# Optimization experiments

Hardware: AMD Instinct MI355X
Metric: run time of the kernel (lower is better)

The kernel has to match this reference:

```python
import jax, jax.numpy as jnp
import numpy as np

EPS = 1e-8
LN_EPS = 1e-5
CAPACITY_BETA = 1.5
IDEAL_CLASSES = 5.0

B, F, E, H, C, G = 8192, 1024, 30, 256, 100, 4096


def setup_inputs() -> dict:
    key = jax.random.key(0)
    ks = jax.random.split(key, 8)
    x = jax.random.normal(ks[0], (B, F), dtype=jnp.float32)
    prototypes = jax.random.normal(ks[1], (E, F), dtype=jnp.float32)
    g_new = jax.random.normal(ks[2], (G,), dtype=jnp.float32)
    g_mem = jax.random.normal(ks[3], (E, G), dtype=jnp.float32)
    class_counts = jax.random.randint(ks[4], (E,), 0, 12, dtype=jnp.int32)
    W1 = jax.random.normal(ks[5], (E, F, H), dtype=jnp.float32) * (1.0 / np.sqrt(F))
    b1 = jnp.zeros((E, H), dtype=jnp.float32)
    gamma = jnp.ones((E, H), dtype=jnp.float32)
    beta = jnp.zeros((E, H), dtype=jnp.float32)
    W2 = jax.random.normal(ks[6], (E, H, C), dtype=jnp.float32) * (1.0 / np.sqrt(H))
    b2 = jnp.zeros((E, C), dtype=jnp.float32)
    return {"x": x, "prototypes": prototypes, "g_new": g_new, "g_mem": g_mem,
            "class_counts": class_counts, "W1": W1, "b1": b1, "gamma": gamma,
            "beta": beta, "W2": W2, "b2": b2}


def _route_scores(x, prototypes, g_new, g_mem, class_counts):
    # Cosine similarity of each sample to each expert prototype: [B, E]
    xn = x / (jnp.linalg.norm(x, axis=-1, keepdims=True) + EPS)
    pn = prototypes / (jnp.linalg.norm(prototypes, axis=-1, keepdims=True) + EPS)
    sim = xn @ pn.T
    # Gradient alignment score per expert (cosine of new grad vs EMA memory), mapped to [0, 1]
    gn = g_new / (jnp.linalg.norm(g_new) + EPS)
    gm = g_mem / (jnp.linalg.norm(g_mem, axis=-1, keepdims=True) + EPS)
    align = 0.5 * (1.0 + gm @ gn)  # [E]
    # Capacity penalty: exponential decay once an expert exceeds its ideal class load
    overload = jnp.maximum(class_counts.astype(jnp.float32) / IDEAL_CLASSES - 1.0, 0.0)
    capacity = jnp.exp(-CAPACITY_BETA * overload)  # [E]
    return sim * (align * capacity)[None, :]  # [B, E]


def reference(x, prototypes, g_new, g_mem, class_counts, W1, b1, gamma, beta, W2, b2):
    scores = _route_scores(x, prototypes, g_new, g_mem, class_counts)  # [B, E]
    assign = jnp.argmax(scores, axis=-1)  # [B] expert id per sample
    # Expert MLP: Linear -> LayerNorm -> GELU -> Linear, evaluated for all experts
    h = jnp.einsum('bf,efh->ebh', x, W1) + b1[:, None, :]  # [E, B, H]
    mu = h.mean(axis=-1, keepdims=True)
    var = ((h - mu) ** 2).mean(axis=-1, keepdims=True)
    ln = (h - mu) * jax.lax.rsqrt(var + LN_EPS) * gamma[:, None, :] + beta[:, None, :]
    a = jax.nn.gelu(ln, approximate=False)  # torch nn.GELU default is exact erf
    logits_all = jnp.einsum('ebh,ehc->ebc', a, W2) + b2[:, None, :]  # [E, B, C]
    # Dispatch: each sample keeps only its assigned expert's logits
    logits = logits_all[assign, jnp.arange(x.shape[0])]  # [B, C]
    return logits
```

## Files before the change

### kernel.cpp

```cpp
#include <hip/hip_runtime.h>
#include <hip/hip_bf16.h>
#include <math.h>
#include <float.h>

namespace {
constexpr int Bn = 8192;
constexpr int Fn = 1024;
constexpr int En = 30;
constexpr int Hn = 256;
constexpr int Cn = 100;
constexpr int Gn = 4096;
constexpr int TILECAP64 = 158;
constexpr int TILECAP16 = 540;
constexpr float EPSF  = 1e-8f;
constexpr float LNEPS = 1e-5f;

typedef _Float16 f16x8 __attribute__((ext_vector_type(8)));
typedef __fp16   h16x2 __attribute__((ext_vector_type(2)));
typedef float    f32x4 __attribute__((ext_vector_type(4)));

__device__ __forceinline__ int bswz(int k) { return (k & 7) ^ ((k >> 3) << 2); }

__device__ __forceinline__ f16x8 pk8(const float* v) {
  union { h16x2 h2[4]; f16x8 v8; } u;
#pragma unroll
  for (int i = 0; i < 4; i++)
    u.h2[i] = __builtin_amdgcn_cvt_pkrtz(v[2 * i], v[2 * i + 1]);
  return u.v8;
}
}

#define GLDS16(g, s) __builtin_amdgcn_global_load_lds(                         \
    (const __attribute__((address_space(1))) void*)(uintptr_t)(g),             \
    (__attribute__((address_space(3))) void*)(uintptr_t)(s), 16, 0, 0)

__global__ __launch_bounds__(256) void k_route_w(
    const float* __restrict__ protos,
    const float* __restrict__ g_new,
    const float* __restrict__ g_mem,
    const int* __restrict__ ccounts,
    float* __restrict__ w,
    int* __restrict__ cnt) {
  const int e = blockIdx.x, t = threadIdx.x;
  if (e == 0 && t < 32) cnt[t] = 0;
  float d = 0.f, gm2 = 0.f, gn2 = 0.f, p2 = 0.f;
  for (int g = t; g < Gn; g += 256) {
    float a = g_new[g];
    float m = g_mem[(size_t)e * Gn + g];
    d += a * m; gm2 += m * m; gn2 += a * a;
  }
  for (int f = t; f < Fn; f += 256) {
    float v = protos[(size_t)e * Fn + f];
    p2 += v * v;
  }
#pragma unroll
  for (int m = 1; m < 64; m <<= 1) {
    d   += __shfl_xor(d, m);
    gm2 += __shfl_xor(gm2, m);
    gn2 += __shfl_xor(gn2, m);
    p2  += __shfl_xor(p2, m);
  }
  __shared__ float red[4][4];
  const int lane = t & 63, wid = t >> 6;
  if (lane == 0) { red[wid][0] = d; red[wid][1] = gm2; red[wid][2] = gn2; red[wid][3] = p2; }
  __syncthreads();
  if (t == 0) {
    d   = red[0][0] + red[1][0] + red[2][0] + red[3][0];
    gm2 = red[0][1] + red[1][1] + red[2][1] + red[3][1];
    gn2 = red[0][2] + red[1][2] + red[2][2] + red[3][2];
    p2  = red[0][3] + red[1][3] + red[2][3] + red[3][3];
    float align = 0.5f * (1.0f + d / ((sqrtf(gm2) + EPSF) * (sqrtf(gn2) + EPSF)));
    float over  = fmaxf((float)ccounts[e] / 5.0f - 1.0f, 0.0f);
    float cap   = expf(-1.5f * over);
    w[e] = align * cap / (sqrtf(p2) + EPSF);
  }
}

__global__ __launch_bounds__(256) void k_scores_mfma(
    const float* __restrict__ x,
    const float* __restrict__ protos,
    const float* __restrict__ w,
    int* __restrict__ assign,
    float* __restrict__ hbuf) {
  const int b0 = blockIdx.x * 16;
  extern __shared__ char smem[];
  __shared__ float av_[16][2];
  __shared__ int   ai_[16][2];
  const int t = threadIdx.x, l = t & 63, wv = t >> 6;
  const int nt = wv & 1;

  {
    float* hz = hbuf + (size_t)blockIdx.x * 4096 + t * 4;
#pragma unroll
    for (int k = 0; k < 4; k++)
      *(float4*)(hz + k * 1024) = make_float4(0.f, 0.f, 0.f, 0.f);
  }

  const char* asrc;
  {
    const int row = t >> 4, pos = t & 15;
    asrc = (const char*)x + (size_t)(b0 + row) * 4096 + (pos ^ (row & 7)) * 16;
  }
  const char* bsrc[2];
#pragma unroll
  for (int i = 0; i < 2; i++) {
    const int D = i * 256 + t, row = D >> 4, pos = D & 15;
    bsrc[i] = (const char*)protos + (size_t)min(row, En - 1) * 4096 +
              (pos ^ (row & 7)) * 16;
  }

  const int r15 = l & 15, kq = l >> 4;
  int addrA[2][2];
#pragma unroll
  for (int ks = 0; ks < 2; ks++)
#pragma unroll
    for (int i = 0; i < 2; i++)
      addrA[ks][i] = r15 * 256 + (((ks * 8 + kq * 2 + i) ^ (r15 & 7)) * 16);
  int addrB[2][2];
#pragma unroll
  for (int ks = 0; ks < 2; ks++)
#pragma unroll
    for (int i = 0; i < 2; i++) {
      const int er = nt * 16 + r15;
      addrB[ks][i] = 4096 + er * 256 + (((ks * 8 + kq * 2 + i) ^ (er & 7)) * 16);
    }

  const int  e_w   = nt * 16 + r15;
  const bool valid = (e_w < En);
  const float wsc  = w[min(e_w, En - 1)];

  f32x4 acc = (f32x4){0.f, 0.f, 0.f, 0.f};

  auto stage = [&](int buf, int kt) {
    char* bb = smem + buf * 12288;
    GLDS16(asrc + kt * 256, bb + wv * 1024);
#pragma unroll
    for (int i = 0; i < 2; i++)
      GLDS16(bsrc[i] + kt * 256, bb + 4096 + i * 4096 + wv * 1024);
  };

  stage(0, 0);
  __syncthreads();
  int cur = 0;
  for (int kt = 0; kt < 16; ++kt) {
    if (kt < 15) stage(cur ^ 1, kt + 1);
    const char* bb = smem + cur * 12288;
    if (wv < 2) {
#pragma unroll
      for (int ks = 0; ks < 2; ks++) {
        f16x8 ah, al;
        {
          float4 a0 = *(const float4*)(bb + addrA[ks][0]);
          float4 a1 = *(const float4*)(bb + addrA[ks][1]);
          float av[8] = {a0.x, a0.y, a0.z, a0.w, a1.x, a1.y, a1.z, a1.w};
#pragma unroll
          for (int j = 0; j < 8; j++) {
            _Float16 hh = (_Float16)av[j];
            ah[j] = hh;
            al[j] = (_Float16)(av[j] - (float)hh);
          }
        }
        f16x8 bh, bl;
        {
          float4 b0v = *(const float4*)(bb + addrB[ks][0]);
          float4 b1v = *(const float4*)(bb + addrB[ks][1]);
          float bv[8] = {b0v.x, b0v.y, b0v.z, b0v.w, b1v.x, b1v.y, b1v.z, b1v.w};
#pragma unroll
          for (int j = 0; j < 8; j++) {
            _Float16 hh = (_Float16)bv[j];
            bh[j] = hh;
            bl[j] = (_Float16)(bv[j] - (float)hh);
          }
        }
        acc = __builtin_amdgcn_mfma_f32_16x16x32_f16(ah, bh, acc, 0, 0, 0);
        acc = __builtin_amdgcn_mfma_f32_16x16x32_f16(al, bh, acc, 0, 0, 0);
        acc = __builtin_amdgcn_mfma_f32_16x16x32_f16(ah, bl, acc, 0, 0, 0);
        acc = __builtin_amdgcn_mfma_f32_16x16x32_f16(al, bl, acc, 0, 0, 0);
      }
    }
    __syncthreads();
    cur ^= 1;
  }

  if (wv < 2) {
#pragma unroll
    for (int j = 0; j < 4; j++) {
      float best = valid ? acc[j] * wsc : -FLT_MAX;
      int bi = e_w;
#pragma unroll
      for (int m = 1; m < 16; m <<= 1) {
        float ov = __shfl_xor(best, m);
        int   oi = __shfl_xor(bi, m);
        if (ov > best || (ov == best && oi < bi)) { best = ov; bi = oi; }
      }
      if (r15 == 0) {
        const int s = kq * 4 + j;
        av_[s][nt] = best;
        ai_[s][nt] = bi;
      }
    }
  }
  __syncthreads();
  if (t < 16) {
    const float v0 = av_[t][0], v1 = av_[t][1];
    assign[b0 + t] = (v1 > v0) ? ai_[t][1] : ai_[t][0];
  }
}

__global__ __launch_bounds__(256) void k_bucket(
    const int* __restrict__ assign,
    int* __restrict__ cnt,
    int* __restrict__ list) {
  __shared__ int lcnt[32], lbase[32];
  const int t = threadIdx.x;
  const int b = blockIdx.x * 256 + t;
  if (t < 32) lcnt[t] = 0;
  __syncthreads();
  const int e = assign[b];
  const int lpos = atomicAdd(&lcnt[e], 1);
  __syncthreads();
  if (t < 32) lbase[t] = (lcnt[t] > 0) ? atomicAdd(&cnt[t], lcnt[t]) : 0;
  __syncthreads();
  list[e * Bn + lbase[e] + lpos] = b;
}

__global__ void k_plan(const int* __restrict__ cnt,
                       int* __restrict__ tiles64,
                       int* __restrict__ tiles16) {
  const int t = threadIdx.x;
  if (t == 0) {
    int tot = 0;
    for (int e = 0; e < En; e++) {
      int nt = (cnt[e] + 63) >> 6;
      for (int k = 0; k < nt && tot + k < TILECAP64; k++)
        tiles64[tot + k] = (e << 16) | k;
      tot += nt;
    }
    for (int k = tot; k < TILECAP64; k++) tiles64[k] = -1;
  } else if (t == 1) {
    int tot = 0;
    for (int e = 0; e < En; e++) {
      int nt = (cnt[e] + 15) >> 4;
      for (int k = 0; k < nt && tot + k < TILECAP16; k++)
        tiles16[tot + k] = (e << 16) | k;
      tot += nt;
    }
    for (int k = tot; k < TILECAP16; k++) tiles16[k] = -1;
  }
}

__global__ __launch_bounds__(256) void k_l1_f16(
    const float* __restrict__ x,
    const float* __restrict__ W1,
    const float* __restrict__ b1,
    const int* __restrict__ cnt,
    const int* __restrict__ list,
    const int* __restrict__ tiles,
    float* __restrict__ hbuf) {
  const int tv = tiles[blockIdx.x];
  if (tv < 0) return;
  const int e = tv >> 16, ti = tv & 0xffff;
  const int n = cnt[e];
  const int s0 = ti * 64;
  const int ns = min(64, n - s0);
  const int h0 = blockIdx.y * 128;
  const int k0 = blockIdx.z * 16;

  extern __shared__ char smem[];
  __shared__ int idx[64];
  const int t = threadIdx.x, l = t & 63, w = t >> 6;
  if (t < 64) idx[t] = list[e * Bn + s0 + min(t, ns - 1)];
  __syncthreads();

  const char* asrc[2];
#pragma unroll
  for (int i = 0; i < 2; i++) {
    const int D = i * 256 + t, row = D >> 3, pos = D & 7;
    asrc[i] = (const char*)x + (size_t)idx[row] * 4096 + (pos ^ (row & 7)) * 16;
  }
  const char* bsrc[4];
#pragma unroll
  for (int i = 0; i < 4; i++) {
    const int k  = i * 8 + w * 2 + (l >> 5);
    const int c  = (l & 31) ^ bswz(k);
    bsrc[i] = (const char*)W1 +
              ((size_t)(e * Fn + k) * Hn + h0) * 4 + c * 16;
  }

  const int r15 = l & 15, kq = l >> 4;
  int addrA[4][2];
#pragma unroll
  for (int m = 0; m < 4; m++)
#pragma unroll
    for (int i = 0; i < 2; i++) {
      const int row = m * 16 + r15;
      addrA[m][i] = row * 128 + (((kq * 2 + i) ^ (row & 7)) * 16);
    }
  int addrB[2][8];
#pragma unroll
  for (int nn = 0; nn < 2; nn++)
#pragma unroll
    for (int j = 0; j < 8; j++) {
      const int h = w * 32 + nn * 16 + r15;
      const int kl = kq * 8 + j;
      addrB[nn][j] = 8192 + kl * 512 + (((h >> 2) ^ bswz(kl)) * 16) + (h & 3) * 4;
    }

  f32x4 acc[4][2];
#pragma unroll
  for (int m = 0; m < 4; m++)
#pragma unroll
    for (int nn = 0; nn < 2; nn++) acc[m][nn] = (f32x4){0.f, 0.f, 0.f, 0.f};

  auto stage = [&](int buf, int kt) {
    char* bb = smem + buf * 24576;
#pragma unroll
    for (int i = 0; i < 2; i++)
      GLDS16(asrc[i] + kt * 128, bb + i * 4096 + w * 1024);
#pragma unroll
    for (int i = 0; i < 4; i++)
      GLDS16(bsrc[i] + (size_t)kt * 32768, bb + 8192 + i * 4096 + w * 1024);
  };

  stage(0, k0);
  __syncthreads();
  int cur = 0;
  for (int kt = k0; kt < k0 + 16; ++kt) {
    if (kt < k0 + 15) stage(cur ^ 1, kt + 1);
    const char* bb = smem + cur * 24576;

    f16x8 ah[4], al[4];
#pragma unroll
    for (int m = 0; m < 4; m++) {
      float4 a0 = *(const float4*)(bb + addrA[m][0]);
      float4 a1 = *(const float4*)(bb + addrA[m][1]);
      float av[8] = {a0.x, a0.y, a0.z, a0.w, a1.x, a1.y, a1.z, a1.w};
#pragma unroll
      for (int j = 0; j < 8; j++) {
        _Float16 hh = (_Float16)av[j];
        ah[m][j] = hh;
        al[m][j] = (_Float16)(av[j] - (float)hh);
      }
    }
#pragma unroll
    for (int nn = 0; nn < 2; nn++) {
      float bv[8];
#pragma unroll
      for (int j = 0; j < 8; j++)
        bv[j] = *(const float*)(bb + addrB[nn][j]);
      const f16x8 bh = pk8(bv);
#pragma unroll
      for (int m = 0; m < 4; m++) {
        acc[m][nn] = __builtin_amdgcn_mfma_f32_16x16x32_f16(ah[m], bh, acc[m][nn], 0, 0, 0);
        acc[m][nn] = __builtin_amdgcn_mfma_f32_16x16x32_f16(al[m], bh, acc[m][nn], 0, 0, 0);
      }
    }
    __syncthreads();
    cur ^= 1;
  }

  float bias[2];
#pragma unroll
  for (int nn = 0; nn < 2; nn++)
    bias[nn] = (blockIdx.z == 0)
             ? b1[(size_t)e * Hn + h0 + w * 32 + nn * 16 + r15] : 0.f;
#pragma unroll
  for (int m = 0; m < 4; m++) {
#pragma unroll
    for (int j = 0; j < 4; j++) {
      const int r = m * 16 + kq * 4 + j;
      if (r < ns) {
        float* dst = hbuf + (size_t)idx[r] * Hn + h0 + w * 32;
#pragma unroll
        for (int nn = 0; nn < 2; nn++)
          atomicAdd(dst + nn * 16 + r15, acc[m][nn][j] + bias[nn]);
      }
    }
  }
}

__global__ __launch_bounds__(256) void k_ln2_mfma(
    const float* __restrict__ hbuf,
    const float* __restrict__ gamma,
    const float* __restrict__ beta,
    const float* __restrict__ W2,
    const float* __restrict__ b2,
    const int* __restrict__ cnt,
    const int* __restrict__ list,
    const int* __restrict__ tiles16,
    float* __restrict__ out) {
  const int tv = tiles16[blockIdx.x];
  if (tv < 0) return;
  const int e = tv >> 16, ti = tv & 0xffff;
  const int n = cnt[e];
  const int s0 = ti * 16;
  const int ns = min(16, n - s0);

  __shared__ __align__(16) char aT[16 * 1024];
  __shared__ __align__(16) char bW[2][13312];
  __shared__ int idx[16];

  const int t = threadIdx.x, l = t & 63, w = t >> 6;
  if (t < 16) idx[t] = list[e * Bn + s0 + min(t, ns - 1)];

  const char* w2e = (const char*)W2 + (size_t)e * (Hn * Cn * 4);
  auto stageB = [&](int buf, int kt) {
    const int base = kt * 12800;
    for (int i = w; i < 13; i += 4) {
      int off = base + i * 1024 + l * 16;
      if (off > 102400 - 16) off = 102400 - 16;
      GLDS16(w2e + off, bW[buf] + i * 1024);
    }
  };

  stageB(0, 0);
  __syncthreads();

  const int s = t >> 4, seg = t & 15;
  const int b = idx[s];
  float hv[16];
  float sum = 0.f, sq = 0.f;
  {
    const float* src = hbuf + (size_t)b * Hn + seg * 16;
#pragma unroll
    for (int i = 0; i < 16; i += 4) {
      float4 v = *(const float4*)(src + i);
      hv[i] = v.x; hv[i+1] = v.y; hv[i+2] = v.z; hv[i+3] = v.w;
      sum += v.x + v.y + v.z + v.w;
      sq  += v.x*v.x + v.y*v.y + v.z*v.z + v.w*v.w;
    }
  }
#pragma unroll
  for (int m = 1; m < 16; m <<= 1) { sum += __shfl_xor(sum, m); sq += __shfl_xor(sq, m); }
  const float mu = sum * (1.f / 256.f);
  float var = fmaxf(sq * (1.f / 256.f) - mu * mu, 0.f);
  const float rstd = rsqrtf(var + LNEPS);
#pragma unroll
  for (int i4 = 0; i4 < 4; i4++) {
    float av[4];
#pragma unroll
    for (int j = 0; j < 4; j++) {
      const int hh = seg * 16 + i4 * 4 + j;
      const float g  = gamma[(size_t)e * Hn + hh];
      const float be = beta[(size_t)e * Hn + hh];
      const float ln = (hv[i4 * 4 + j] - mu) * rstd * g + be;
      av[j] = 0.5f * ln * (1.0f + erff(ln * 0.70710678118654752f));
    }
    const int chunk = (seg * 4 + i4) ^ (s & 7);
    *(float4*)(aT + s * 1024 + chunk * 16) = make_float4(av[0], av[1], av[2], av[3]);
  }

  const int r15 = l & 15, kq = l >> 4;
  int addrB[2][8];
#pragma unroll
  for (int ni = 0; ni < 2; ni++) {
    const int nt = w + ni * 4;
    const int c = nt * 16 + r15;
#pragma unroll
    for (int j = 0; j < 8; j++)
      addrB[ni][j] = ((kq * 8 + j) * Cn + c) * 4;
  }

  f32x4 acc[2];
  acc[0] = (f32x4){0.f, 0.f, 0.f, 0.f};
  acc[1] = (f32x4){0.f, 0.f, 0.f, 0.f};

  __syncthreads();

  int cur = 0;
  for (int kt = 0; kt < 8; ++kt) {
    if (kt < 7) stageB(cur ^ 1, kt + 1);

    f16x8 ah, al;
    {
      const int c0 = (kt * 8 + kq * 2) ^ (r15 & 7);
      const int c1 = (kt * 8 + kq * 2 + 1) ^ (r15 & 7);
      float4 a0 = *(const float4*)(aT + r15 * 1024 + c0 * 16);
      float4 a1 = *(const float4*)(aT + r15 * 1024 + c1 * 16);
      float av[8] = {a0.x, a0.y, a0.z, a0.w, a1.x, a1.y, a1.z, a1.w};
#pragma unroll
      for (int j = 0; j < 8; j++) {
        _Float16 hh = (_Float16)av[j];
        ah[j] = hh;
        al[j] = (_Float16)(av[j] - (float)hh);
      }
    }
#pragma unroll
    for (int ni = 0; ni < 2; ni++) {
      const int nt = w + ni * 4;
      if (nt < 7) {
        float bv[8];
#pragma unroll
        for (int j = 0; j < 8; j++)
          bv[j] = *(const float*)(bW[cur] + addrB[ni][j]);
        f16x8 bh, bl;
#pragma unroll
        for (int j = 0; j < 8; j++) {
          _Float16 hh = (_Float16)bv[j];
          bh[j] = hh;
          bl[j] = (_Float16)(bv[j] - (float)hh);
        }
        acc[ni] = __builtin_amdgcn_mfma_f32_16x16x32_f16(ah, bh, acc[ni], 0, 0, 0);
        acc[ni] = __builtin_amdgcn_mfma_f32_16x16x32_f16(al, bh, acc[ni], 0, 0, 0);
        acc[ni] = __builtin_amdgcn_mfma_f32_16x16x32_f16(ah, bl, acc[ni], 0, 0, 0);
      }
    }
    __syncthreads();
    cur ^= 1;
  }

#pragma unroll
  for (int ni = 0; ni < 2; ni++) {
    const int nt = w + ni * 4;
    if (nt >= 7) continue;
    const int c = nt * 16 + r15;
    if (c >= Cn) continue;
    const float bias = b2[(size_t)e * Cn + c];
#pragma unroll
    for (int j = 0; j < 4; j++) {
      const int r = kq * 4 + j;
      if (r < ns)
        out[(size_t)idx[r] * Cn + c] = acc[ni][j] + bias;
    }
  }
}

extern "C" void kernel_launch(void* const* d_in, const int* in_sizes, int n_in,
                              void* d_out, int out_size, void* d_ws, size_t ws_size,
                              hipStream_t stream) {
  const void* x       = d_in[0];
  const void* protos  = d_in[1];
  const void* g_new   = d_in[2];
  const void* g_mem   = d_in[3];
  const int*  ccounts = (const int*)d_in[4];
  const void* W1      = d_in[5];
  const void* b1      = d_in[6];
  const void* gamma   = d_in[7];
  const void* beta    = d_in[8];
  const void* W2      = d_in[9];
  const void* b2      = d_in[10];

  char* ws = (char*)d_ws;
  float* w       = (float*)(ws);
  int*   assign  = (int*)(ws + 512);
  int*   tiles64 = (int*)(ws + 512);
  int*   tiles16 = (int*)(ws + 512 + 1024);
  int*   cnt     = (int*)(ws + 512 + Bn * 4);
  int*   list    = (int*)(ws + 512 + Bn * 4 + 256);
  float* hbuf    = (float*)(ws + 1016576);

  k_route_w<<<dim3(En), 256, 0, stream>>>(
      (const float*)protos, (const float*)g_new, (const float*)g_mem,
      ccounts, w, cnt);
  k_scores_mfma<<<dim3(Bn / 16), 256, 24576, stream>>>(
      (const float*)x, (const float*)protos, w, assign, hbuf);
  k_bucket<<<Bn / 256, 256, 0, stream>>>(assign, cnt, list);
  k_plan<<<1, 64, 0, stream>>>(cnt, tiles64, tiles16);
  k_l1_f16<<<dim3(TILECAP64, 2, 2), 256, 49152, stream>>>(
      (const float*)x, (const float*)W1, (const float*)b1,
      cnt, list, tiles64, hbuf);
  k_ln2_mfma<<<dim3(TILECAP16), 256, 0, stream>>>(
      hbuf, (const float*)gamma, (const float*)beta, (const float*)W2,
      (const float*)b2, cnt, list, tiles16, (float*)d_out);
}
```

Baseline: 219.3 us.

## Fuse bucketing into scores kernel and split K across all four waves

The scores kernel now uses all four waves by splitting the feature dimension into two halves, each processed by a pair of waves, with a shared-memory reduction of the partial accumulators before the argmax. The separate bucketing kernel is removed: each block appends its 16 samples to per-expert lists with local and global atomics directly after computing assignments. This cuts one launch and the assign buffer round-trip and halves the serial K loop per block, at the cost of twice the shared memory per block (lower occupancy) and more global atomics on cnt, since there are far more blocks.

```diff
diff --git a/kernel.cpp b/kernel.cpp
--- a/kernel.cpp
+++ b/kernel.cpp
@@ -80,14 +80,19 @@
     const float* __restrict__ x,
     const float* __restrict__ protos,
     const float* __restrict__ w,
-    int* __restrict__ assign,
+    int* __restrict__ cnt,
+    int* __restrict__ list,
     float* __restrict__ hbuf) {
   const int b0 = blockIdx.x * 16;
   extern __shared__ char smem[];
   __shared__ float av_[16][2];
   __shared__ int   ai_[16][2];
+  __shared__ float pacc[2][64][4];
+  __shared__ int   lcnt[32], lbase[32];
   const int t = threadIdx.x, l = t & 63, wv = t >> 6;
-  const int nt = wv & 1;
+  const int nt = wv & 1, kh = wv >> 1;
+
+  if (t < 32) lcnt[t] = 0;
 
   {
     float* hz = hbuf + (size_t)blockIdx.x * 4096 + t * 4;
@@ -110,19 +115,21 @@
   }
 
   const int r15 = l & 15, kq = l >> 4;
+  const int khb = kh * 12288;
   int addrA[2][2];
 #pragma unroll
   for (int ks = 0; ks < 2; ks++)
 #pragma unroll
     for (int i = 0; i < 2; i++)
-      addrA[ks][i] = r15 * 256 + (((ks * 8 + kq * 2 + i) ^ (r15 & 7)) * 16);
+      addrA[ks][i] = khb + r15 * 256 + (((ks * 8 + kq * 2 + i) ^ (r15 & 7)) * 16);
   int addrB[2][2];
 #pragma unroll
   for (int ks = 0; ks < 2; ks++)
 #pragma unroll
     for (int i = 0; i < 2; i++) {
       const int er = nt * 16 + r15;
-      addrB[ks][i] = 4096 + er * 256 + (((ks * 8 + kq * 2 + i) ^ (er & 7)) * 16);
+      addrB[ks][i] = khb + 4096 + er * 256 +
+                     (((ks * 8 + kq * 2 + i) ^ (er & 7)) * 16);
     }
 
   const int  e_w   = nt * 16 + r15;
@@ -132,57 +139,67 @@
   f32x4 acc = (f32x4){0.f, 0.f, 0.f, 0.f};
 
   auto stage = [&](int buf, int kt) {
-    char* bb = smem + buf * 12288;
-    GLDS16(asrc + kt * 256, bb + wv * 1024);
+    char* bb = smem + buf * 24576;
+    const int ko = kt * 256;
+    GLDS16(asrc + ko,            bb + wv * 1024);
 #pragma unroll
     for (int i = 0; i < 2; i++)
-      GLDS16(bsrc[i] + kt * 256, bb + 4096 + i * 4096 + wv * 1024);
+      GLDS16(bsrc[i] + ko,       bb + 4096 + i * 4096 + wv * 1024);
+    GLDS16(asrc + 2048 + ko,     bb + 12288 + wv * 1024);
+#pragma unroll
+    for (int i = 0; i < 2; i++)
+      GLDS16(bsrc[i] + 2048 + ko, bb + 12288 + 4096 + i * 4096 + wv * 1024);
   };
 
   stage(0, 0);
   __syncthreads();
   int cur = 0;
-  for (int kt = 0; kt < 16; ++kt) {
-    if (kt < 15) stage(cur ^ 1, kt + 1);
-    const char* bb = smem + cur * 12288;
-    if (wv < 2) {
-#pragma unroll
-      for (int ks = 0; ks < 2; ks++) {
-        f16x8 ah, al;
-        {
-          float4 a0 = *(const float4*)(bb + addrA[ks][0]);
-          float4 a1 = *(const float4*)(bb + addrA[ks][1]);
-          float av[8] = {a0.x, a0.y, a0.z, a0.w, a1.x, a1.y, a1.z, a1.w};
-#pragma unroll
-          for (int j = 0; j < 8; j++) {
-            _Float16 hh = (_Float16)av[j];
-            ah[j] = hh;
-            al[j] = (_Float16)(av[j] - (float)hh);
-          }
+  for (int kt = 0; kt < 8; ++kt) {
+    if (kt < 7) stage(cur ^ 1, kt + 1);
+    const char* bb = smem + cur * 24576;
+#pragma unroll
+    for (int ks = 0; ks < 2; ks++) {
+      f16x8 ah, al;
+      {
+        float4 a0 = *(const float4*)(bb + addrA[ks][0]);
+        float4 a1 = *(const float4*)(bb + addrA[ks][1]);
+        float av[8] = {a0.x, a0.y, a0.z, a0.w, a1.x, a1.y, a1.z, a1.w};
+#pragma unroll
+        for (int j = 0; j < 8; j++) {
+          _Float16 hh = (_Float16)av[j];
+          ah[j] = hh;
+          al[j] = (_Float16)(av[j] - (float)hh);
         }
-        f16x8 bh, bl;
-        {
-          float4 b0v = *(const float4*)(bb + addrB[ks][0]);
-          float4 b1v = *(const float4*)(bb + addrB[ks][1]);
-          float bv[8] = {b0v.x, b0v.y, b0v.z, b0v.w, b1v.x, b1v.y, b1v.z, b1v.w};
-#pragma unroll
-          for (int j = 0; j < 8; j++) {
-            _Float16 hh = (_Float16)bv[j];
-            bh[j] = hh;
-            bl[j] = (_Float16)(bv[j] - (float)hh);
-          }
+      }
+      f16x8 bh, bl;
+      {
+        float4 b0v = *(const float4*)(bb + addrB[ks][0]);
+        float4 b1v = *(const float4*)(bb + addrB[ks][1]);
+        float bv[8] = {b0v.x, b0v.y, b0v.z, b0v.w, b1v.x, b1v.y, b1v.z, b1v.w};
+#pragma unroll
+        for (int j = 0; j < 8; j++) {
+          _Float16 hh = (_Float16)bv[j];
+          bh[j] = hh;
+          bl[j] = (_Float16)(bv[j] - (float)hh);
         }
-        acc = __builtin_amdgcn_mfma_f32_16x16x32_f16(ah, bh, acc, 0, 0, 0);
-        acc = __builtin_amdgcn_mfma_f32_16x16x32_f16(al, bh, acc, 0, 0, 0);
-        acc = __builtin_amdgcn_mfma_f32_16x16x32_f16(ah, bl, acc, 0, 0, 0);
-        acc = __builtin_amdgcn_mfma_f32_16x16x32_f16(al, bl, acc, 0, 0, 0);
-      }
+      }
+      acc = __builtin_amdgcn_mfma_f32_16x16x32_f16(ah, bh, acc, 0, 0, 0);
+      acc = __builtin_amdgcn_mfma_f32_16x16x32_f16(al, bh, acc, 0, 0, 0);
+      acc = __builtin_amdgcn_mfma_f32_16x16x32_f16(ah, bl, acc, 0, 0, 0);
+      acc = __builtin_amdgcn_mfma_f32_16x16x32_f16(al, bl, acc, 0, 0, 0);
     }
     __syncthreads();
     cur ^= 1;
   }
 
-  if (wv < 2) {
+  if (kh == 1) {
+#pragma unroll
+    for (int j = 0; j < 4; j++) pacc[nt][l][j] = acc[j];
+  }
+  __syncthreads();
+  if (kh == 0) {
+#pragma unroll
+    for (int j = 0; j < 4; j++) acc[j] += pacc[nt][l][j];
 #pragma unroll
     for (int j = 0; j < 4; j++) {
       float best = valid ? acc[j] * wsc : -FLT_MAX;
@@ -201,27 +218,18 @@
     }
   }
   __syncthreads();
+
+  int myE = -1, lpos = 0;
   if (t < 16) {
     const float v0 = av_[t][0], v1 = av_[t][1];
-    assign[b0 + t] = (v1 > v0) ? ai_[t][1] : ai_[t][0];
-  }
-}
-
-__global__ __launch_bounds__(256) void k_bucket(
-    const int* __restrict__ assign,
-    int* __restrict__ cnt,
-    int* __restrict__ list) {
-  __shared__ int lcnt[32], lbase[32];
-  const int t = threadIdx.x;
-  const int b = blockIdx.x * 256 + t;
-  if (t < 32) lcnt[t] = 0;
-  __syncthreads();
-  const int e = assign[b];
-  const int lpos = atomicAdd(&lcnt[e], 1);
+    myE = (v1 > v0) ? ai_[t][1] : ai_[t][0];
+    lpos = atomicAdd(&lcnt[myE], 1);
+  }
   __syncthreads();
   if (t < 32) lbase[t] = (lcnt[t] > 0) ? atomicAdd(&cnt[t], lcnt[t]) : 0;
   __syncthreads();
-  list[e * Bn + lbase[e] + lpos] = b;
+  if (t < 16)
+    list[myE * Bn + lbase[myE] + lpos] = b0 + t;
 }
 
 __global__ void k_plan(const int* __restrict__ cnt,
@@ -542,7 +550,6 @@
 
   char* ws = (char*)d_ws;
   float* w       = (float*)(ws);
-  int*   assign  = (int*)(ws + 512);
   int*   tiles64 = (int*)(ws + 512);
   int*   tiles16 = (int*)(ws + 512 + 1024);
   int*   cnt     = (int*)(ws + 512 + Bn * 4);
@@ -552,9 +559,8 @@
   k_route_w<<<dim3(En), 256, 0, stream>>>(
       (const float*)protos, (const float*)g_new, (const float*)g_mem,
       ccounts, w, cnt);
-  k_scores_mfma<<<dim3(Bn / 16), 256, 24576, stream>>>(
-      (const float*)x, (const float*)protos, w, assign, hbuf);
-  k_bucket<<<Bn / 256, 256, 0, stream>>>(assign, cnt, list);
+  k_scores_mfma<<<dim3(Bn / 16), 256, 49152, stream>>>(
+      (const float*)x, (const float*)protos, w, cnt, list, hbuf);
   k_plan<<<1, 64, 0, stream>>>(cnt, tiles64, tiles16);
   k_l1_f16<<<dim3(TILECAP64, 2, 2), 256, 49152, stream>>>(
       (const float*)x, (const float*)W1, (const float*)b1,
```

Result: faster. 210.8 us (-3.9%).
